# Kernel tuning notes

Hardware: AMD Instinct MI355X
Metric: run time of the kernel (lower is better)

The kernel has to match this reference:

```python
import jax, jax.numpy as jnp
import numpy as np

TEXT_DIM, GIN = 5000, 128
B, N, E = 4096, 200000, 6400000
AE_HID, AE_EMB, G_HID, G_EMB = 8, 4, 8, 4


def _gcn(x, W, b, src, dst):
    N_ = x.shape[0]
    h = x @ W
    loop = jnp.arange(N_)
    s = jnp.concatenate([src, loop])
    d = jnp.concatenate([dst, loop])
    deg = jax.ops.segment_sum(jnp.ones(s.shape[0], h.dtype), d, num_segments=N_)
    dinv = jnp.where(deg > 0, jax.lax.rsqrt(jnp.maximum(deg, 1e-12)), 0.0)
    norm = dinv[s] * dinv[d]
    out = jax.ops.segment_sum(h[s] * norm[:, None], d, num_segments=N_)
    return out + b


def setup_inputs() -> dict:
    key = jax.random.key(0)
    ks = jax.random.split(key, 20)
    def lin(k, fan_in, fan_out):
        lim = 1.0 / np.sqrt(fan_in)
        kw, kb = jax.random.split(k)
        W = jax.random.uniform(kw, (fan_in, fan_out), jnp.float32, -lim, lim)
        b = jax.random.uniform(kb, (fan_out,), jnp.float32, -lim, lim)
        return W, b
    W_e1, b_e1 = lin(ks[0], TEXT_DIM, AE_HID)
    W_e2, b_e2 = lin(ks[1], AE_HID, AE_EMB)
    W_d1, b_d1 = lin(ks[2], AE_EMB, AE_HID)
    W_d2, b_d2 = lin(ks[3], AE_HID, TEXT_DIM)
    W_g1, b_g1 = lin(ks[4], GIN, G_HID)
    W_g2, b_g2 = lin(ks[5], G_HID, G_EMB)
    W_c, b_c = lin(ks[6], AE_EMB + G_EMB, 1)
    text_x = jax.random.normal(ks[7], (B, TEXT_DIM), jnp.float32)
    node_x = jax.random.normal(ks[8], (N, GIN), jnp.float32)
    edge_index = jax.random.randint(ks[9], (2, E), 0, N, jnp.int64 if jax.config.jax_enable_x64 else jnp.int32)
    batch = jnp.sort(jax.random.randint(ks[10], (N,), 0, B, edge_index.dtype))
    return {"text_x": text_x, "node_x": node_x, "edge_index": edge_index, "batch": batch,
            "W_e1": W_e1, "b_e1": b_e1, "W_e2": W_e2, "b_e2": b_e2,
            "W_d1": W_d1, "b_d1": b_d1, "W_d2": W_d2, "b_d2": b_d2,
            "W_g1": W_g1, "b_g1": b_g1, "W_g2": W_g2, "b_g2": b_g2,
            "W_c": W_c, "b_c": b_c}


def reference(text_x, node_x, edge_index, batch,
              W_e1, b_e1, W_e2, b_e2, W_d1, b_d1, W_d2, b_d2,
              W_g1, b_g1, W_g2, b_g2, W_c, b_c):
    # Autoencoder (eval mode: dropout = identity)
    z_text = jax.nn.relu(jax.nn.relu(text_x @ W_e1 + b_e1) @ W_e2 + b_e2)
    x_hat = jax.nn.sigmoid(jax.nn.relu(z_text @ W_d1 + b_d1) @ W_d2 + b_d2)
    # GNN encoder
    src, dst = edge_index[0], edge_index[1]
    h = jax.nn.relu(_gcn(node_x, W_g1, b_g1, src, dst))
    h = _gcn(h, W_g2, b_g2, src, dst)
    # global mean pool over graphs
    nb = text_x.shape[0]
    sums = jax.ops.segment_sum(h, batch, num_segments=nb)
    cnt = jax.ops.segment_sum(jnp.ones(h.shape[0], h.dtype), batch, num_segments=nb)
    z_graph = sums / jnp.maximum(cnt, 1.0)[:, None]
    z = jnp.concatenate([z_text, z_graph], axis=1)
    logits = z @ W_c + b_c
    return (x_hat, logits, z)
```

## Files before the change

kernel.cpp:

```cpp
#include <hip/hip_runtime.h>

#define BB 4096
#define TD 5000
#define NN 200000
#define EE 6400000
#define NBK 782
#define WS_NEED 66488188ull

__global__ void k_init(const int* __restrict__ e, unsigned int* __restrict__ deg,
                       int* __restrict__ flag) {
    int i = blockIdx.x * 256 + threadIdx.x;
    if (i < NN) deg[i] = 1u;
    if (blockIdx.x == 0) {
        __shared__ int r[256];
        int tid = threadIdx.x;
        int acc = 0;
        for (int k = tid; k < 4096; k += 256) acc |= e[2 * k + 1];
        r[tid] = acc;
        __syncthreads();
        for (int s = 128; s > 0; s >>= 1) {
            if (tid < s) r[tid] |= r[tid + s];
            __syncthreads();
        }
        if (tid == 0) *flag = (r[0] == 0) ? 1 : 0;
    }
}

__device__ void role_rank(int rid, int tid, const int* __restrict__ edge,
                          const int* __restrict__ flag, unsigned int* __restrict__ deg,
                          unsigned int* __restrict__ rnk) {
    int f = *flag;
    int base = rid * 2048 + tid;
    int d[8];
#pragma unroll
    for (int k = 0; k < 8; k++) {
        int e = base + k * 256;
        d[k] = f ? edge[2 * (EE + e)] : edge[EE + e];
    }
    unsigned int rr[8];
#pragma unroll
    for (int k = 0; k < 8; k++) rr[k] = atomicAdd(&deg[d[k]], 1u);
#pragma unroll
    for (int k = 0; k < 8; k++) rnk[base + k * 256] = rr[k];
}

__device__ void role_enc(int row, int tid, const float* __restrict__ text,
                         const float* __restrict__ We1, const float* __restrict__ be1,
                         const float* __restrict__ We2, const float* __restrict__ be2,
                         float* __restrict__ z_text) {
    __shared__ float red[8][256];
    __shared__ float t1[8];
    const float4* xrow = (const float4*)(text + (size_t)row * TD);
    float acc[8];
#pragma unroll
    for (int j = 0; j < 8; j++) acc[j] = 0.f;
    for (int v = tid; v < 1250; v += 256) {
        float4 xv = xrow[v];
        const float4* w = (const float4*)(We1 + (size_t)v * 32);
        float xc[4] = {xv.x, xv.y, xv.z, xv.w};
#pragma unroll
        for (int c = 0; c < 4; c++) {
            float4 wa = w[c * 2], wb = w[c * 2 + 1];
            acc[0] += xc[c] * wa.x; acc[1] += xc[c] * wa.y;
            acc[2] += xc[c] * wa.z; acc[3] += xc[c] * wa.w;
            acc[4] += xc[c] * wb.x; acc[5] += xc[c] * wb.y;
            acc[6] += xc[c] * wb.z; acc[7] += xc[c] * wb.w;
        }
    }
#pragma unroll
    for (int j = 0; j < 8; j++) red[j][tid] = acc[j];
    __syncthreads();
    for (int s = 128; s > 0; s >>= 1) {
        if (tid < s) {
#pragma unroll
            for (int j = 0; j < 8; j++) red[j][tid] += red[j][tid + s];
        }
        __syncthreads();
    }
    if (tid < 8) t1[tid] = fmaxf(red[tid][0] + be1[tid], 0.f);
    __syncthreads();
    if (tid < 4) {
        float z = be2[tid];
#pragma unroll
        for (int k = 0; k < 8; k++) z += t1[k] * We2[k * 4 + tid];
        z_text[row * 4 + tid] = fmaxf(z, 0.f);
    }
}

__device__ void role_mm(int mid, int tid, const float* __restrict__ nodex,
                        const float* __restrict__ Wg1, float* __restrict__ h0g) {
    __shared__ float W[1024];
    for (int i = tid; i < 1024; i += 256) W[i] = Wg1[i];
    __syncthreads();
    int row = mid * 256 + tid;
    if (row >= NN) return;
    const float4* xr = (const float4*)(nodex + (size_t)row * 128);
    float acc[8];
#pragma unroll
    for (int j = 0; j < 8; j++) acc[j] = 0.f;
#pragma unroll 8
    for (int c = 0; c < 32; c++) {
        float4 v = xr[c];
        const float* wr = &W[c * 32];
#pragma unroll
        for (int j = 0; j < 8; j++)
            acc[j] += v.x * wr[j] + v.y * wr[8 + j] + v.z * wr[16 + j] + v.w * wr[24 + j];
    }
    float* o = h0g + (size_t)row * 8;
#pragma unroll
    for (int j = 0; j < 8; j++) o[j] = acc[j];
}

__device__ void role_place(int pid, int tid, const int* __restrict__ edge,
                           const int* __restrict__ flag, const unsigned int* __restrict__ indptr,
                           const unsigned int* __restrict__ rnk, int* __restrict__ csr) {
    int f = *flag;
    int base = pid * 1024 + tid;
    int s[4], d[4];
#pragma unroll
    for (int k = 0; k < 4; k++) {
        int e = base + k * 256;
        s[k] = f ? edge[2 * e] : edge[e];
        d[k] = f ? edge[2 * (EE + e)] : edge[EE + e];
    }
    unsigned int rr[4];
#pragma unroll
    for (int k = 0; k < 4; k++) rr[k] = rnk[base + k * 256];
    unsigned int ip[4];
#pragma unroll
    for (int k = 0; k < 4; k++) ip[k] = indptr[d[k]];
#pragma unroll
    for (int k = 0; k < 4; k++) csr[ip[k] + rr[k] - 1u] = s[k];
}

__device__ void role_scale(int sid, int tid, float* __restrict__ h0g,
                           const float* __restrict__ dinv) {
    int i = sid * 256 + tid;
    if (i >= NN) return;
    float di = dinv[i];
    float4* p = (float4*)(h0g + (size_t)i * 8);
    float4 a = p[0], b = p[1];
    a.x *= di; a.y *= di; a.z *= di; a.w *= di;
    b.x *= di; b.y *= di; b.z *= di; b.w *= di;
    p[0] = a; p[1] = b;
}

__device__ void role_decode(int row, int tid, const float* __restrict__ zsrc, int zstride,
                            const float* __restrict__ Wd1, const float* __restrict__ bd1,
                            const float* __restrict__ Wd2, const float* __restrict__ bd2,
                            float* __restrict__ xhat) {
    float zz[4];
#pragma unroll
    for (int j = 0; j < 4; j++) zz[j] = zsrc[row * zstride + j];
    float t[8];
#pragma unroll
    for (int k = 0; k < 8; k++) {
        float s = bd1[k];
#pragma unroll
        for (int j = 0; j < 4; j++) s += zz[j] * Wd1[j * 8 + k];
        t[k] = fmaxf(s, 0.f);
    }
    float4* orow = (float4*)(xhat + (size_t)row * TD);
    for (int c4 = tid; c4 < 1250; c4 += 256) {
        float4 s = *(const float4*)(bd2 + c4 * 4);
#pragma unroll
        for (int k = 0; k < 8; k++) {
            float4 w = *(const float4*)(Wd2 + (size_t)k * TD + c4 * 4);
            s.x += t[k] * w.x; s.y += t[k] * w.y;
            s.z += t[k] * w.z; s.w += t[k] * w.w;
        }
        s.x = 1.f / (1.f + expf(-s.x));
        s.y = 1.f / (1.f + expf(-s.y));
        s.z = 1.f / (1.f + expf(-s.z));
        s.w = 1.f / (1.f + expf(-s.w));
        orow[c4] = s;
    }
}

__global__ __launch_bounds__(256) void k_fat1(
    const int* __restrict__ edge, const int* __restrict__ flag,
    unsigned int* __restrict__ deg, unsigned int* __restrict__ rnk,
    const float* __restrict__ text,
    const float* __restrict__ We1, const float* __restrict__ be1,
    const float* __restrict__ We2, const float* __restrict__ be2,
    float* __restrict__ z_text,
    const float* __restrict__ nodex, const float* __restrict__ Wg1,
    float* __restrict__ h0g)
{
    int bid = blockIdx.x, tid = threadIdx.x;
    if (bid < 6250) {
        if (bid & 1) role_enc(bid >> 1, tid, text, We1, be1, We2, be2, z_text);
        else role_rank(bid >> 1, tid, edge, flag, deg, rnk);
    } else if (bid < 7221) {
        role_enc(3125 + (bid - 6250), tid, text, We1, be1, We2, be2, z_text);
    } else {
        role_mm(bid - 7221, tid, nodex, Wg1, h0g);
    }
}

__global__ __launch_bounds__(256) void k_fat2(
    const int* __restrict__ edge, const int* __restrict__ flag,
    const unsigned int* __restrict__ indptr, const unsigned int* __restrict__ rnk,
    int* __restrict__ csr, float* __restrict__ h0g, const float* __restrict__ dinv,
    const float* __restrict__ zsrc, int zstride,
    const float* __restrict__ Wd1, const float* __restrict__ bd1,
    const float* __restrict__ Wd2, const float* __restrict__ bd2,
    float* __restrict__ xhat, int ndec)
{
    int bid = blockIdx.x, tid = threadIdx.x;
    if (ndec > 0) {
        if (bid < 8192) {
            if (bid & 1) role_decode(bid >> 1, tid, zsrc, zstride, Wd1, bd1, Wd2, bd2, xhat);
            else role_place(bid >> 1, tid, edge, flag, indptr, rnk, csr);
        } else if (bid < 10346) {
            role_place(4096 + (bid - 8192), tid, edge, flag, indptr, rnk, csr);
        } else {
            role_scale(bid - 10346, tid, h0g, dinv);
        }
    } else {
        if (bid < 6250) role_place(bid, tid, edge, flag, indptr, rnk, csr);
        else role_scale(bid - 6250, tid, h0g, dinv);
    }
}

__global__ __launch_bounds__(256) void k_dec(
    const float* __restrict__ zsrc, int zstride,
    const float* __restrict__ Wd1, const float* __restrict__ bd1,
    const float* __restrict__ Wd2, const float* __restrict__ bd2,
    float* __restrict__ xhat)
{
    role_decode(blockIdx.x, threadIdx.x, zsrc, zstride, Wd1, bd1, Wd2, bd2, xhat);
}

__global__ void kA_all(const unsigned int* __restrict__ deg, float* __restrict__ dinv,
                       unsigned int* __restrict__ bsum, const int* __restrict__ batch,
                       const int* __restrict__ flag, unsigned int* __restrict__ bnd) {
    __shared__ unsigned int s[256];
    int tid = threadIdx.x;
    int i = blockIdx.x * 256 + tid;
    unsigned int c = 0u;
    if (i < NN) {
        unsigned int u = deg[i];
        dinv[i] = rsqrtf((float)u);
        c = u - 1u;
        int fg = *flag;
        int b = fg ? batch[2 * i] : batch[i];
        int bp = (i == 0) ? -1 : (fg ? batch[2 * (i - 1)] : batch[i - 1]);
        for (int bb = bp + 1; bb <= b; bb++) bnd[bb] = (unsigned int)i;
        if (i == NN - 1)
            for (int bb = b + 1; bb <= BB; bb++) bnd[bb] = (unsigned int)NN;
    }
    s[tid] = c;
    __syncthreads();
    for (int st = 128; st > 0; st >>= 1) {
        if (tid < st) s[tid] += s[tid + st];
        __syncthreads();
    }
    if (tid == 0) bsum[blockIdx.x] = s[0];
}

__global__ void kB_scanblocks(const unsigned int* __restrict__ bsum, unsigned int* __restrict__ bpre,
                              unsigned int* __restrict__ indptr) {
    __shared__ unsigned int s[1024];
    int t = threadIdx.x;
    s[t] = (t < NBK) ? bsum[t] : 0u;
    __syncthreads();
    for (int off = 1; off < 1024; off <<= 1) {
        unsigned int v = (t >= off) ? s[t - off] : 0u;
        __syncthreads();
        s[t] += v;
        __syncthreads();
    }
    if (t < NBK) bpre[t] = (t == 0) ? 0u : s[t - 1];
    if (t == 0) indptr[NN] = EE;
}

__global__ void kC_indptr(const unsigned int* __restrict__ deg, const unsigned int* __restrict__ bpre,
                          unsigned int* __restrict__ indptr) {
    __shared__ unsigned int s[256];
    int tid = threadIdx.x;
    int i = blockIdx.x * 256 + tid;
    unsigned int c = (i < NN) ? (deg[i] - 1u) : 0u;
    s[tid] = c;
    __syncthreads();
    for (int off = 1; off < 256; off <<= 1) {
        unsigned int v = (tid >= off) ? s[tid - off] : 0u;
        __syncthreads();
        s[tid] += v;
        __syncthreads();
    }
    if (i < NN) indptr[i] = bpre[blockIdx.x] + s[tid] - c;
}

__global__ __launch_bounds__(256) void k_gather1(
    const unsigned int* __restrict__ indptr, const int* __restrict__ csr_src,
    const float* __restrict__ h0g, const float* __restrict__ dinv,
    const float* __restrict__ bg1, const float* __restrict__ Wg2,
    float* __restrict__ h2g)
{
    __shared__ float W[32];
    __shared__ float b1[8];
    __shared__ float h1s[4][8];
    int tid = threadIdx.x;
    if (tid < 32) W[tid] = Wg2[tid];
    if (tid < 8) b1[tid] = bg1[tid];
    __syncthreads();
    int wid = tid >> 6, lane = tid & 63;
    int i = blockIdx.x * 4 + wid;
    if (i < NN) {
        int beg = indptr[i], end = indptr[i + 1];
        int f = lane & 7;
        float a = 0.f;
        for (int k = beg + (lane >> 3); k < end; k += 8)
            a += h0g[(size_t)csr_src[k] * 8 + f];
        a += __shfl_xor(a, 8, 64);
        a += __shfl_xor(a, 16, 64);
        a += __shfl_xor(a, 32, 64);
        if (lane < 8) {
            float di = dinv[i];
            h1s[wid][f] = fmaxf(di * (a + h0g[(size_t)i * 8 + f]) + b1[f], 0.f);
        }
    }
    __syncthreads();
    if (i < NN && lane < 4) {
        float di = dinv[i];
        float s = 0.f;
#pragma unroll
        for (int k = 0; k < 8; k++) s += h1s[wid][k] * W[k * 4 + lane];
        h2g[(size_t)i * 4 + lane] = di * s;
    }
}

__global__ __launch_bounds__(256) void k_gather2(
    const unsigned int* __restrict__ indptr, const int* __restrict__ csr_src,
    const float* __restrict__ h2g, const float* __restrict__ dinv,
    const float* __restrict__ bg2, float* __restrict__ h2f)
{
    __shared__ float b2[4];
    int tid = threadIdx.x;
    if (tid < 4) b2[tid] = bg2[tid];
    __syncthreads();
    int wid = tid >> 6, lane = tid & 63;
    int i = blockIdx.x * 4 + wid;
    if (i >= NN) return;
    int beg = indptr[i], end = indptr[i + 1];
    int f = lane & 3;
    float a = 0.f;
    for (int k = beg + (lane >> 2); k < end; k += 16)
        a += h2g[(size_t)csr_src[k] * 4 + f];
    a += __shfl_xor(a, 4, 64);
    a += __shfl_xor(a, 8, 64);
    a += __shfl_xor(a, 16, 64);
    a += __shfl_xor(a, 32, 64);
    if (lane < 4) {
        float di = dinv[i];
        h2f[(size_t)i * 4 + f] = di * (a + h2g[(size_t)i * 4 + f]) + b2[f];
    }
}

__global__ __launch_bounds__(256) void k_final(
    const float* __restrict__ h2f, const unsigned int* __restrict__ bnd,
    const float* __restrict__ z_text, const float* __restrict__ Wc,
    const float* __restrict__ bc, float* __restrict__ out_logits,
    float* __restrict__ out_z)
{
    __shared__ float red[256][4];
    int g = blockIdx.x, tid = threadIdx.x;
    int lo = bnd[g], hi = bnd[g + 1];
    float a0 = 0.f, a1 = 0.f, a2 = 0.f, a3 = 0.f;
    for (int i = lo + tid; i < hi; i += 256) {
        float4 v = *(const float4*)(h2f + (size_t)i * 4);
        a0 += v.x; a1 += v.y; a2 += v.z; a3 += v.w;
    }
    red[tid][0] = a0; red[tid][1] = a1; red[tid][2] = a2; red[tid][3] = a3;
    __syncthreads();
    for (int s = 128; s > 0; s >>= 1) {
        if (tid < s) {
            red[tid][0] += red[tid + s][0]; red[tid][1] += red[tid + s][1];
            red[tid][2] += red[tid + s][2]; red[tid][3] += red[tid + s][3];
        }
        __syncthreads();
    }
    if (tid == 0) {
        float c = (float)(hi - lo);
        c = fmaxf(c, 1.f);
        float z8[8];
#pragma unroll
        for (int j = 0; j < 4; j++) z8[j] = z_text[g * 4 + j];
#pragma unroll
        for (int j = 0; j < 4; j++) z8[4 + j] = red[0][j] / c;
        float l = bc[0];
#pragma unroll
        for (int k = 0; k < 8; k++) l += z8[k] * Wc[k];
        out_logits[g] = l;
#pragma unroll
        for (int k = 0; k < 8; k++) out_z[g * 8 + k] = z8[k];
    }
}

extern "C" void kernel_launch(void* const* d_in, const int* in_sizes, int n_in,
                              void* d_out, int out_size, void* d_ws, size_t ws_size,
                              hipStream_t stream) {
    const float* text  = (const float*)d_in[0];
    const float* nodex = (const float*)d_in[1];
    const int* edge    = (const int*)d_in[2];
    const int* batch   = (const int*)d_in[3];
    const float* We1 = (const float*)d_in[4];
    const float* be1 = (const float*)d_in[5];
    const float* We2 = (const float*)d_in[6];
    const float* be2 = (const float*)d_in[7];
    const float* Wd1 = (const float*)d_in[8];
    const float* bd1 = (const float*)d_in[9];
    const float* Wd2 = (const float*)d_in[10];
    const float* bd2 = (const float*)d_in[11];
    const float* Wg1 = (const float*)d_in[12];
    const float* bg1 = (const float*)d_in[13];
    const float* Wg2 = (const float*)d_in[14];
    const float* bg2 = (const float*)d_in[15];
    const float* Wc  = (const float*)d_in[16];
    const float* bc  = (const float*)d_in[17];

    const bool use_ws = (ws_size >= WS_NEED);
    char* sc = use_ws ? (char*)d_ws : (char*)d_out;

    float*        h0g    = (float*)(sc + 0);
    float*        h2g    = (float*)(sc + 6400000);
    float*        h2f    = (float*)(sc + 9600000);
    float*        dinv   = (float*)(sc + 12800000);
    unsigned int* deg    = (unsigned int*)(sc + 13600000);
    unsigned int* indptr = (unsigned int*)(sc + 14400000);
    unsigned int* rnk    = (unsigned int*)(sc + 15200004);
    int*          csr    = (int*)(sc + 40800004);
    unsigned int* bsum   = (unsigned int*)(sc + 66400004);
    unsigned int* bpre   = (unsigned int*)(sc + 66403132);
    float*        z_text = (float*)(sc + 66406260);
    unsigned int* bnd    = (unsigned int*)(sc + 66471796);
    int*          flag   = (int*)(sc + 66488184);

    float* out_xhat   = (float*)d_out;
    float* out_logits = out_xhat + (size_t)BB * TD;
    float* out_z      = out_logits + BB;

    k_init<<<NBK, 256, 0, stream>>>(edge, deg, flag);
    k_fat1<<<8003, 256, 0, stream>>>(edge, flag, deg, rnk,
                                     text, We1, be1, We2, be2, z_text,
                                     nodex, Wg1, h0g);
    kA_all<<<NBK, 256, 0, stream>>>(deg, dinv, bsum, batch, flag, bnd);
    kB_scanblocks<<<1, 1024, 0, stream>>>(bsum, bpre, indptr);
    kC_indptr<<<NBK, 256, 0, stream>>>(deg, bpre, indptr);

    if (use_ws) {
        k_fat2<<<11128, 256, 0, stream>>>(edge, flag, indptr, rnk, csr, h0g, dinv,
                                          z_text, 4, Wd1, bd1, Wd2, bd2, out_xhat, 4096);
    } else {
        k_fat2<<<7032, 256, 0, stream>>>(edge, flag, indptr, rnk, csr, h0g, dinv,
                                         (const float*)nullptr, 0, Wd1, bd1, Wd2, bd2,
                                         (float*)nullptr, 0);
    }

    k_gather1<<<(NN + 3) / 4, 256, 0, stream>>>(indptr, csr, h0g, dinv, bg1, Wg2, h2g);
    k_gather2<<<(NN + 3) / 4, 256, 0, stream>>>(indptr, csr, h2g, dinv, bg2, h2f);
    k_final<<<BB, 256, 0, stream>>>(h2f, bnd, z_text, Wc, bc, out_logits, out_z);

    if (!use_ws) {
        k_dec<<<BB, 256, 0, stream>>>(out_z, 8, Wd1, bd1, Wd2, bd2, out_xhat);
    }
}
```

Before: 739.6 us.

## Fold dinv scaling into node matmul and co-schedule decoder with first gather

The node feature matmul moves from the first fat kernel into the second, where dinv is already available, so the scale is applied at write time and the separate scale pass is removed. The decoder blocks are now interleaved with the first GCN gather instead of with the CSR placement. Temporary rank, degree and block-sum buffers are placed in the output region, which lowers the workspace requirement and lets more configurations take the workspace path. This changes which memory-bound phases overlap, and it relies on the decoder overwriting that scratch in x_hat only after those buffers are dead.

```diff
diff --git a/kernel.cpp b/kernel.cpp
--- a/kernel.cpp
+++ b/kernel.cpp
@@ -5,7 +5,7 @@
 #define NN 200000
 #define EE 6400000
 #define NBK 782
-#define WS_NEED 66488188ull
+#define WS_NEED 40081932ull
 
 __global__ void k_init(const int* __restrict__ e, unsigned int* __restrict__ deg,
                        int* __restrict__ flag) {
@@ -88,7 +88,8 @@
 }
 
 __device__ void role_mm(int mid, int tid, const float* __restrict__ nodex,
-                        const float* __restrict__ Wg1, float* __restrict__ h0g) {
+                        const float* __restrict__ Wg1, const float* __restrict__ dinv,
+                        float* __restrict__ h0g) {
     __shared__ float W[1024];
     for (int i = tid; i < 1024; i += 256) W[i] = Wg1[i];
     __syncthreads();
@@ -106,9 +107,10 @@
         for (int j = 0; j < 8; j++)
             acc[j] += v.x * wr[j] + v.y * wr[8 + j] + v.z * wr[16 + j] + v.w * wr[24 + j];
     }
+    float di = dinv[row];
     float* o = h0g + (size_t)row * 8;
 #pragma unroll
-    for (int j = 0; j < 8; j++) o[j] = acc[j];
+    for (int j = 0; j < 8; j++) o[j] = di * acc[j];
 }
 
 __device__ void role_place(int pid, int tid, const int* __restrict__ edge,
@@ -133,18 +135,6 @@
     for (int k = 0; k < 4; k++) csr[ip[k] + rr[k] - 1u] = s[k];
 }
 
-__device__ void role_scale(int sid, int tid, float* __restrict__ h0g,
-                           const float* __restrict__ dinv) {
-    int i = sid * 256 + tid;
-    if (i >= NN) return;
-    float di = dinv[i];
-    float4* p = (float4*)(h0g + (size_t)i * 8);
-    float4 a = p[0], b = p[1];
-    a.x *= di; a.y *= di; a.z *= di; a.w *= di;
-    b.x *= di; b.y *= di; b.z *= di; b.w *= di;
-    p[0] = a; p[1] = b;
-}
-
 __device__ void role_decode(int row, int tid, const float* __restrict__ zsrc, int zstride,
                             const float* __restrict__ Wd1, const float* __restrict__ bd1,
                             const float* __restrict__ Wd2, const float* __restrict__ bd2,
@@ -174,6 +164,42 @@
         s.z = 1.f / (1.f + expf(-s.z));
         s.w = 1.f / (1.f + expf(-s.w));
         orow[c4] = s;
+    }
+}
+
+__device__ void role_g1(int gid, int tid, const unsigned int* __restrict__ indptr,
+                        const int* __restrict__ csr, const float* __restrict__ h0g,
+                        const float* __restrict__ dinv, const float* __restrict__ bg1,
+                        const float* __restrict__ Wg2, float* __restrict__ h2g) {
+    __shared__ float W[32];
+    __shared__ float b1[8];
+    __shared__ float h1s[4][8];
+    if (tid < 32) W[tid] = Wg2[tid];
+    if (tid < 8) b1[tid] = bg1[tid];
+    __syncthreads();
+    int wid = tid >> 6, lane = tid & 63;
+    int i = gid * 4 + wid;
+    if (i < NN) {
+        int beg = indptr[i], end = indptr[i + 1];
+        int f = lane & 7;
+        float a = 0.f;
+        for (int k = beg + (lane >> 3); k < end; k += 8)
+            a += h0g[(size_t)csr[k] * 8 + f];
+        a += __shfl_xor(a, 8, 64);
+        a += __shfl_xor(a, 16, 64);
+        a += __shfl_xor(a, 32, 64);
+        if (lane < 8) {
+            float di = dinv[i];
+            h1s[wid][f] = fmaxf(di * (a + h0g[(size_t)i * 8 + f]) + b1[f], 0.f);
+        }
+    }
+    __syncthreads();
+    if (i < NN && lane < 4) {
+        float di = dinv[i];
+        float s = 0.f;
+#pragma unroll
+        for (int k = 0; k < 8; k++) s += h1s[wid][k] * W[k * 4 + lane];
+        h2g[(size_t)i * 4 + lane] = di * s;
     }
 }
 
@@ -183,53 +209,64 @@
     const float* __restrict__ text,
     const float* __restrict__ We1, const float* __restrict__ be1,
     const float* __restrict__ We2, const float* __restrict__ be2,
-    float* __restrict__ z_text,
-    const float* __restrict__ nodex, const float* __restrict__ Wg1,
-    float* __restrict__ h0g)
+    float* __restrict__ z_text)
 {
     int bid = blockIdx.x, tid = threadIdx.x;
     if (bid < 6250) {
         if (bid & 1) role_enc(bid >> 1, tid, text, We1, be1, We2, be2, z_text);
         else role_rank(bid >> 1, tid, edge, flag, deg, rnk);
-    } else if (bid < 7221) {
+    } else {
         role_enc(3125 + (bid - 6250), tid, text, We1, be1, We2, be2, z_text);
-    } else {
-        role_mm(bid - 7221, tid, nodex, Wg1, h0g);
     }
 }
 
 __global__ __launch_bounds__(256) void k_fat2(
     const int* __restrict__ edge, const int* __restrict__ flag,
     const unsigned int* __restrict__ indptr, const unsigned int* __restrict__ rnk,
-    int* __restrict__ csr, float* __restrict__ h0g, const float* __restrict__ dinv,
-    const float* __restrict__ zsrc, int zstride,
-    const float* __restrict__ Wd1, const float* __restrict__ bd1,
-    const float* __restrict__ Wd2, const float* __restrict__ bd2,
-    float* __restrict__ xhat, int ndec)
+    int* __restrict__ csr, const float* __restrict__ nodex,
+    const float* __restrict__ Wg1, const float* __restrict__ dinv,
+    float* __restrict__ h0g)
 {
     int bid = blockIdx.x, tid = threadIdx.x;
-    if (ndec > 0) {
-        if (bid < 8192) {
-            if (bid & 1) role_decode(bid >> 1, tid, zsrc, zstride, Wd1, bd1, Wd2, bd2, xhat);
-            else role_place(bid >> 1, tid, edge, flag, indptr, rnk, csr);
-        } else if (bid < 10346) {
-            role_place(4096 + (bid - 8192), tid, edge, flag, indptr, rnk, csr);
-        } else {
-            role_scale(bid - 10346, tid, h0g, dinv);
-        }
-    } else {
-        if (bid < 6250) role_place(bid, tid, edge, flag, indptr, rnk, csr);
-        else role_scale(bid - 6250, tid, h0g, dinv);
-    }
-}
-
-__global__ __launch_bounds__(256) void k_dec(
-    const float* __restrict__ zsrc, int zstride,
+    if (bid < 6250) role_place(bid, tid, edge, flag, indptr, rnk, csr);
+    else role_mm(bid - 6250, tid, nodex, Wg1, dinv, h0g);
+}
+
+__global__ __launch_bounds__(256) void k_g1(
+    const unsigned int* __restrict__ indptr, const int* __restrict__ csr,
+    const float* __restrict__ h0g, const float* __restrict__ dinv,
+    const float* __restrict__ bg1, const float* __restrict__ Wg2,
+    float* __restrict__ h2g)
+{
+    role_g1(blockIdx.x, threadIdx.x, indptr, csr, h0g, dinv, bg1, Wg2, h2g);
+}
+
+__global__ __launch_bounds__(256) void k_g1_ws(
+    const unsigned int* __restrict__ indptr, const int* __restrict__ csr,
+    const float* __restrict__ h0g, const float* __restrict__ dinv,
+    const float* __restrict__ bg1, const float* __restrict__ Wg2,
+    float* __restrict__ h2g,
+    const float* __restrict__ z_text,
     const float* __restrict__ Wd1, const float* __restrict__ bd1,
     const float* __restrict__ Wd2, const float* __restrict__ bd2,
     float* __restrict__ xhat)
 {
-    role_decode(blockIdx.x, threadIdx.x, zsrc, zstride, Wd1, bd1, Wd2, bd2, xhat);
+    int bid = blockIdx.x, tid = threadIdx.x;
+    if (bid < 8192) {
+        if (bid & 1) role_decode(bid >> 1, tid, z_text, 4, Wd1, bd1, Wd2, bd2, xhat);
+        else role_g1(bid >> 1, tid, indptr, csr, h0g, dinv, bg1, Wg2, h2g);
+    } else {
+        role_g1(bid - 4096, tid, indptr, csr, h0g, dinv, bg1, Wg2, h2g);
+    }
+}
+
+__global__ __launch_bounds__(256) void k_dec(
+    const float* __restrict__ zsrc,
+    const float* __restrict__ Wd1, const float* __restrict__ bd1,
+    const float* __restrict__ Wd2, const float* __restrict__ bd2,
+    float* __restrict__ xhat)
+{
+    role_decode(blockIdx.x, threadIdx.x, zsrc, 8, Wd1, bd1, Wd2, bd2, xhat);
 }
 
 __global__ void kA_all(const unsigned int* __restrict__ deg, float* __restrict__ dinv,
@@ -290,45 +327,6 @@
         __syncthreads();
     }
     if (i < NN) indptr[i] = bpre[blockIdx.x] + s[tid] - c;
-}
-
-__global__ __launch_bounds__(256) void k_gather1(
-    const unsigned int* __restrict__ indptr, const int* __restrict__ csr_src,
-    const float* __restrict__ h0g, const float* __restrict__ dinv,
-    const float* __restrict__ bg1, const float* __restrict__ Wg2,
-    float* __restrict__ h2g)
-{
-    __shared__ float W[32];
-    __shared__ float b1[8];
-    __shared__ float h1s[4][8];
-    int tid = threadIdx.x;
-    if (tid < 32) W[tid] = Wg2[tid];
-    if (tid < 8) b1[tid] = bg1[tid];
-    __syncthreads();
-    int wid = tid >> 6, lane = tid & 63;
-    int i = blockIdx.x * 4 + wid;
-    if (i < NN) {
-        int beg = indptr[i], end = indptr[i + 1];
-        int f = lane & 7;
-        float a = 0.f;
-        for (int k = beg + (lane >> 3); k < end; k += 8)
-            a += h0g[(size_t)csr_src[k] * 8 + f];
-        a += __shfl_xor(a, 8, 64);
-        a += __shfl_xor(a, 16, 64);
-        a += __shfl_xor(a, 32, 64);
-        if (lane < 8) {
-            float di = dinv[i];
-            h1s[wid][f] = fmaxf(di * (a + h0g[(size_t)i * 8 + f]) + b1[f], 0.f);
-        }
-    }
-    __syncthreads();
-    if (i < NN && lane < 4) {
-        float di = dinv[i];
-        float s = 0.f;
-#pragma unroll
-        for (int k = 0; k < 8; k++) s += h1s[wid][k] * W[k * 4 + lane];
-        h2g[(size_t)i * 4 + lane] = di * s;
-    }
 }
 
 __global__ __launch_bounds__(256) void k_gather2(
@@ -420,49 +418,69 @@
     const float* Wc  = (const float*)d_in[16];
     const float* bc  = (const float*)d_in[17];
 
-    const bool use_ws = (ws_size >= WS_NEED);
-    char* sc = use_ws ? (char*)d_ws : (char*)d_out;
-
-    float*        h0g    = (float*)(sc + 0);
-    float*        h2g    = (float*)(sc + 6400000);
-    float*        h2f    = (float*)(sc + 9600000);
-    float*        dinv   = (float*)(sc + 12800000);
-    unsigned int* deg    = (unsigned int*)(sc + 13600000);
-    unsigned int* indptr = (unsigned int*)(sc + 14400000);
-    unsigned int* rnk    = (unsigned int*)(sc + 15200004);
-    int*          csr    = (int*)(sc + 40800004);
-    unsigned int* bsum   = (unsigned int*)(sc + 66400004);
-    unsigned int* bpre   = (unsigned int*)(sc + 66403132);
-    float*        z_text = (float*)(sc + 66406260);
-    unsigned int* bnd    = (unsigned int*)(sc + 66471796);
-    int*          flag   = (int*)(sc + 66488184);
-
     float* out_xhat   = (float*)d_out;
     float* out_logits = out_xhat + (size_t)BB * TD;
     float* out_z      = out_logits + BB;
 
+    const bool use_ws = (ws_size >= WS_NEED);
+
+    float *h0g, *h2g, *h2f, *dinv, *z_text;
+    unsigned int *deg, *indptr, *rnk, *bsum, *bpre, *bnd;
+    int *csr, *flag;
+
+    if (use_ws) {
+        char* w = (char*)d_ws;
+        h0g    = (float*)(w + 0);
+        h2g    = (float*)(w + 6400000);
+        h2f    = (float*)(w + 9600000);
+        dinv   = (float*)(w + 12800000);
+        indptr = (unsigned int*)(w + 13600000);
+        csr    = (int*)(w + 14400004);
+        z_text = (float*)(w + 40000004);
+        bnd    = (unsigned int*)(w + 40065540);
+        flag   = (int*)(w + 40081928);
+        char* o = (char*)d_out;
+        rnk  = (unsigned int*)(o + 0);
+        deg  = (unsigned int*)(o + 25600000);
+        bsum = (unsigned int*)(o + 26400000);
+        bpre = (unsigned int*)(o + 26403128);
+    } else {
+        char* o = (char*)d_out;
+        h0g    = (float*)(o + 0);
+        h2g    = (float*)(o + 6400000);
+        h2f    = (float*)(o + 9600000);
+        dinv   = (float*)(o + 12800000);
+        deg    = (unsigned int*)(o + 13600000);
+        indptr = (unsigned int*)(o + 14400000);
+        rnk    = (unsigned int*)(o + 15200004);
+        csr    = (int*)(o + 40800004);
+        bsum   = (unsigned int*)(o + 66400004);
+        bpre   = (unsigned int*)(o + 66403132);
+        z_text = (float*)(o + 66406260);
+        bnd    = (unsigned int*)(o + 66471796);
+        flag   = (int*)(o + 66488184);
+    }
+
     k_init<<<NBK, 256, 0, stream>>>(edge, deg, flag);
-    k_fat1<<<8003, 256, 0, stream>>>(edge, flag, deg, rnk,
-                                     text, We1, be1, We2, be2, z_text,
-                                     nodex, Wg1, h0g);
+    k_fat1<<<7221, 256, 0, stream>>>(edge, flag, deg, rnk,
+                                     text, We1, be1, We2, be2, z_text);
     kA_all<<<NBK, 256, 0, stream>>>(deg, dinv, bsum, batch, flag, bnd);
     kB_scanblocks<<<1, 1024, 0, stream>>>(bsum, bpre, indptr);
     kC_indptr<<<NBK, 256, 0, stream>>>(deg, bpre, indptr);
+    k_fat2<<<7032, 256, 0, stream>>>(edge, flag, indptr, rnk, csr,
+                                     nodex, Wg1, dinv, h0g);
 
     if (use_ws) {
-        k_fat2<<<11128, 256, 0, stream>>>(edge, flag, indptr, rnk, csr, h0g, dinv,
-                                          z_text, 4, Wd1, bd1, Wd2, bd2, out_xhat, 4096);
+        k_g1_ws<<<54096, 256, 0, stream>>>(indptr, csr, h0g, dinv, bg1, Wg2, h2g,
+                                           z_text, Wd1, bd1, Wd2, bd2, out_xhat);
     } else {
-        k_fat2<<<7032, 256, 0, stream>>>(edge, flag, indptr, rnk, csr, h0g, dinv,
-                                         (const float*)nullptr, 0, Wd1, bd1, Wd2, bd2,
-                                         (float*)nullptr, 0);
-    }
-
-    k_gather1<<<(NN + 3) / 4, 256, 0, stream>>>(indptr, csr, h0g, dinv, bg1, Wg2, h2g);
+        k_g1<<<(NN + 3) / 4, 256, 0, stream>>>(indptr, csr, h0g, dinv, bg1, Wg2, h2g);
+    }
+
     k_gather2<<<(NN + 3) / 4, 256, 0, stream>>>(indptr, csr, h2g, dinv, bg2, h2f);
     k_final<<<BB, 256, 0, stream>>>(h2f, bnd, z_text, Wc, bc, out_logits, out_z);
 
     if (!use_ws) {
-        k_dec<<<BB, 256, 0, stream>>>(out_z, 8, Wd1, bd1, Wd2, bd2, out_xhat);
-    }
-}
+        k_dec<<<BB, 256, 0, stream>>>(out_z, Wd1, bd1, Wd2, bd2, out_xhat);
+    }
+}
```

Result: no change. 729.8 us (-1.3%).
